# Kernel tuning notes

Hardware: AMD Instinct MI355X
Metric: run time of the kernel (lower is better)

The kernel has to match this reference:

```python
import jax, jax.numpy as jnp
import numpy as np

NB_VEC = 4  # module init arg nbVec
TEMP = 20.0  # distance temperature in exp(-d/20)


def setup_inputs() -> dict:
    key = jax.random.key(0)
    k1, k2 = jax.random.split(key)
    B, C, H, W = 16, 64, 256, 256
    x = jax.random.normal(k1, (B, C, H, W), dtype=jnp.float32)
    # stands in for torch.rand score init used when prior is None
    score_init = jax.random.uniform(k2, (B, H * W), dtype=jnp.float32)
    return {"x": x, "score_init": score_init}


def reference(x, score_init):
    B, C, H, W = x.shape
    N = H * W
    # [B, N, C] flattened spatial features
    xf = jnp.transpose(x, (0, 2, 3, 1)).reshape(B, N, C)
    batch = jnp.arange(B)
    score = score_init
    vecs, sims = [], []
    for _ in range(NB_VEC):
        ind = jnp.argmax(score, axis=1)                      # [B] greedy pick
        raw = xf[batch, ind]                                 # [B, C]
        d2 = jnp.sum((xf - raw[:, None, :]) ** 2, axis=-1)   # [B, N]
        # safe sqrt (distance is exactly 0 at the selected pixel)
        sim = jnp.exp(-jnp.sqrt(jnp.maximum(d2, 1e-12)) / TEMP)
        simNorm = sim / jnp.sum(sim, axis=1, keepdims=True)
        reprVec = jnp.einsum('bnc,bn->bc', xf, simNorm)      # softmax-weighted agg
        vecs.append(reprVec)
        sims.append(sim.reshape(B, 1, H, W))
        score = (1.0 - sim) * score                          # suppress nearby pts
    vecList = jnp.stack(vecs, axis=1)                        # [B, nbVec, C]
    simList = jnp.concatenate(sims, axis=1)                  # [B, nbVec, H, W]
    # selectedPos is only incremented in the onlySimSample branch; zeros here
    selectedPos = jnp.zeros((B, 1, H, W), dtype=x.dtype)
    return vecList, simList, selectedPos
```

## Files before the change

### kernel.cpp

```cpp
#include <hip/hip_runtime.h>

#define BB 16
#define CC 64
#define NN 65536
#define NBV 4
#define B64 (BB * 64)


__global__ __launch_bounds__(256)
void k_argmax1(const float* __restrict__ sc_in,
               float* __restrict__ bval, int* __restrict__ bidx,
               float* __restrict__ sel_out) {
    int b = blockIdx.y, blk = blockIdx.x, tid = threadIdx.x;
    const float* s = sc_in + (size_t)b * NN + blk * 1024;
    float v = -1e30f; int vi = 0x7fffffff;
    #pragma unroll
    for (int k = 0; k < 4; k++) {
        int idx = k * 256 + tid;
        float xv = s[idx];
        if (xv > v) { v = xv; vi = blk * 1024 + idx; }
    }
    size_t gt = ((size_t)(b * 64 + blk)) * 256 + tid;
    #pragma unroll
    for (int k = 0; k < 4; k++) sel_out[gt + (size_t)k * 262144] = 0.f;
    __shared__ float sv[256]; __shared__ int si[256];
    sv[tid] = v; si[tid] = vi;
    __syncthreads();
    for (int st = 128; st > 0; st >>= 1) {
        if (tid < st) {
            float ov = sv[tid + st]; int oi = si[tid + st];
            if (ov > sv[tid] || (ov == sv[tid] && oi < si[tid])) { sv[tid] = ov; si[tid] = oi; }
        }
        __syncthreads();
    }
    if (tid == 0) { bval[b * 64 + blk] = sv[0]; bidx[b * 64 + blk] = si[0]; }
}

__global__ __launch_bounds__(256, 2)
void k_iter(const float* __restrict__ x, const float* __restrict__ score_in,
            float* __restrict__ score_out,
            float* __restrict__ bval, int* __restrict__ bidx,
            float* __restrict__ wpart, float* __restrict__ sspart,
            float* __restrict__ sim_out, int iter) {
    int b = blockIdx.y, blk = blockIdx.x, tid = threadIdx.x;
    int lane = tid & 63, wv = tid >> 6;
    __shared__ float raw_s[64];
    __shared__ float4 d2p[2][4][64];

    int rb = (iter & 1) * B64, wb = ((iter & 1) ^ 1) * B64;

    if (tid < 64) {
        float v = bval[rb + b * 64 + tid]; int vi = bidx[rb + b * 64 + tid];
        #pragma unroll
        for (int off = 32; off >= 1; off >>= 1) {
            float ov = __shfl_down(v, off, 64); int oi = __shfl_down(vi, off, 64);
            if (ov > v || (ov == v && oi < vi)) { v = ov; vi = oi; }
        }
        int ind = __shfl(vi, 0, 64);
        raw_s[tid] = x[((size_t)b * 64 + tid) * NN + ind];
    }
    __syncthreads();

    const float* xb = x + ((size_t)b * 64 + wv * 16) * NN;
    float raw[16];
    #pragma unroll
    for (int j = 0; j < 16; j++) raw[j] = raw_s[wv * 16 + j];
    float acc[16];
    #pragma unroll
    for (int j = 0; j < 16; j++) acc[j] = 0.f;

    const size_t sb = (size_t)b * NN;
    const size_t simb = (size_t)(b * NBV + iter) * NN;
    const bool w0 = (wv == 0), upd = (iter < 3);

    float ssacc = 0.f, smax = -1e30f; int smaxi = 0;
    float4 sc_next;
    if (w0 && upd) sc_next = *(const float4*)(score_in + sb + blk * 1024 + lane * 4);

    #pragma unroll 1
    for (int g = 0; g < 4; g++) {
        int n0 = blk * 1024 + g * 256 + lane * 4;
        float4 xv[16];
        #pragma unroll
        for (int j = 0; j < 16; j++) xv[j] = *(const float4*)(xb + (size_t)j * NN + n0);
        float4 sc_cur = sc_next;
        if (w0 && upd && g < 3) sc_next = *(const float4*)(score_in + sb + n0 + 256);
        float4 d2 = make_float4(0.f, 0.f, 0.f, 0.f);
        #pragma unroll
        for (int j = 0; j < 16; j++) {
            float r = raw[j];
            float dx = xv[j].x - r, dy = xv[j].y - r, dz = xv[j].z - r, dw = xv[j].w - r;
            d2.x = fmaf(dx, dx, d2.x); d2.y = fmaf(dy, dy, d2.y);
            d2.z = fmaf(dz, dz, d2.z); d2.w = fmaf(dw, dw, d2.w);
        }
        d2p[g & 1][wv][lane] = d2;
        __syncthreads();
        float4 a0 = d2p[g & 1][0][lane], a1 = d2p[g & 1][1][lane];
        float4 a2 = d2p[g & 1][2][lane], a3 = d2p[g & 1][3][lane];
        float4 sim;
        sim.x = expf(-sqrtf(fmaxf((a0.x + a1.x) + (a2.x + a3.x), 1e-12f)) * 0.05f);
        sim.y = expf(-sqrtf(fmaxf((a0.y + a1.y) + (a2.y + a3.y), 1e-12f)) * 0.05f);
        sim.z = expf(-sqrtf(fmaxf((a0.z + a1.z) + (a2.z + a3.z), 1e-12f)) * 0.05f);
        sim.w = expf(-sqrtf(fmaxf((a0.w + a1.w) + (a2.w + a3.w), 1e-12f)) * 0.05f);
        #pragma unroll
        for (int j = 0; j < 16; j++) {
            acc[j] = fmaf(sim.x, xv[j].x, acc[j]);
            acc[j] = fmaf(sim.y, xv[j].y, acc[j]);
            acc[j] = fmaf(sim.z, xv[j].z, acc[j]);
            acc[j] = fmaf(sim.w, xv[j].w, acc[j]);
        }
        if (w0) {
            ssacc += (sim.x + sim.y) + (sim.z + sim.w);
            *(float4*)(sim_out + simb + n0) = sim;
            if (upd) {
                float4 sc;
                sc.x = sc_cur.x * (1.f - sim.x);
                sc.y = sc_cur.y * (1.f - sim.y);
                sc.z = sc_cur.z * (1.f - sim.z);
                sc.w = sc_cur.w * (1.f - sim.w);
                *(float4*)(score_out + sb + n0) = sc;
                if (sc.x > smax) { smax = sc.x; smaxi = n0; }
                if (sc.y > smax) { smax = sc.y; smaxi = n0 + 1; }
                if (sc.z > smax) { smax = sc.z; smaxi = n0 + 2; }
                if (sc.w > smax) { smax = sc.w; smaxi = n0 + 3; }
            }
        }
    }

    #pragma unroll
    for (int j = 0; j < 16; j++) {
        float v = acc[j];
        #pragma unroll
        for (int off = 32; off >= 1; off >>= 1) v += __shfl_down(v, off, 64);
        if (lane == 0) wpart[(((size_t)b * 64) + blk) * 64 + wv * 16 + j] = v;
    }
    if (w0) {
        float v = ssacc;
        #pragma unroll
        for (int off = 32; off >= 1; off >>= 1) v += __shfl_down(v, off, 64);
        if (lane == 0) sspart[b * 64 + blk] = v;
        if (upd) {
            #pragma unroll
            for (int off = 32; off >= 1; off >>= 1) {
                float ov = __shfl_down(smax, off, 64); int oi = __shfl_down(smaxi, off, 64);
                if (ov > smax || (ov == smax && oi < smaxi)) { smax = ov; smaxi = oi; }
            }
            if (lane == 0) { bval[wb + b * 64 + blk] = smax; bidx[wb + b * 64 + blk] = smaxi; }
        }
    }
}

__global__ void k_fin(const float* __restrict__ wpart, const float* __restrict__ sspart,
                      float* __restrict__ vec_out, int iter) {
    int b = blockIdx.x, tid = threadIdx.x;
    float w = 0.f;
    for (int blk = 0; blk < 64; blk++) w += wpart[(((size_t)b * 64) + blk) * 64 + tid];
    float ss = 0.f;
    for (int blk = 0; blk < 64; blk++) ss += sspart[b * 64 + blk];
    vec_out[(b * NBV + iter) * 64 + tid] = w / ss;
}

extern "C" void kernel_launch(void* const* d_in, const int* in_sizes, int n_in,
                              void* d_out, int out_size, void* d_ws, size_t ws_size,
                              hipStream_t stream) {
    const float* x = (const float*)d_in[0];
    const float* sc_in = (const float*)d_in[1];
    float* out = (float*)d_out;
    float* vec_out = out;
    float* sim_out = vec_out + (size_t)BB * NBV * CC;
    float* sel_out = sim_out + (size_t)BB * NBV * NN;

    float* ws = (float*)d_ws;
    float* score = ws;
    float* bval = ws + (size_t)BB * NN;
    int* bidx = (int*)(bval + 2 * B64);
    float* wpart = bval + 4 * B64;
    float* sspart = wpart + (size_t)BB * 64 * 64;

    k_argmax1<<<dim3(64, BB), 256, 0, stream>>>(sc_in, bval, bidx, sel_out);
    for (int it = 0; it < NBV; it++) {
        const float* s_in = (it == 0) ? sc_in : score;
        k_iter<<<dim3(64, BB), 256, 0, stream>>>(x, s_in, score, bval, bidx,
                                                 wpart, sspart, sim_out, it);
        k_fin<<<dim3(BB), 64, 0, stream>>>(wpart, sspart, vec_out, it);
    }
}
```

Before: 548.1 us.

## Give each wave all 64 channels over fewer pixels and widen partial reductions

The iteration kernel now assigns each wave a strip of 128 pixels with all 64 channels held in registers, so distances are computed entirely within a thread and the shared-memory cross-wave d2 exchange and per-group barriers disappear. The grid doubles to 128 blocks per batch, and partial argmax, weight and sum results go up to 512 partitions per batch. The argmax-seeding kernel and the finalize kernel are reworked to produce and consume the larger partition count. The change removes synchronisation and raises parallelism, but each thread now holds 128 floats of x plus 64 accumulators, which may push register pressure and lower occupancy. It also adds 64 wave shuffle reductions per wave and a larger final reduction.

```diff
diff --git a/kernel.cpp b/kernel.cpp
--- a/kernel.cpp
+++ b/kernel.cpp
@@ -4,7 +4,8 @@
 #define CC 64
 #define NN 65536
 #define NBV 4
-#define B64 (BB * 64)
+#define NPART 512
+#define BP (BB * NPART)
 
 
 __global__ __launch_bounds__(256)
@@ -12,28 +13,20 @@
                float* __restrict__ bval, int* __restrict__ bidx,
                float* __restrict__ sel_out) {
     int b = blockIdx.y, blk = blockIdx.x, tid = threadIdx.x;
-    const float* s = sc_in + (size_t)b * NN + blk * 1024;
-    float v = -1e30f; int vi = 0x7fffffff;
+    int lane = tid & 63, wv = tid >> 6;
+    int n0 = blk * 512 + tid * 2;
+    const float* s = sc_in + (size_t)b * NN;
+    float v0 = s[n0], v1 = s[n0 + 1];
+    float v = v0; int vi = n0;
+    if (v1 > v) { v = v1; vi = n0 + 1; }
+    sel_out[(size_t)b * NN + n0] = 0.f;
+    sel_out[(size_t)b * NN + n0 + 1] = 0.f;
     #pragma unroll
-    for (int k = 0; k < 4; k++) {
-        int idx = k * 256 + tid;
-        float xv = s[idx];
-        if (xv > v) { v = xv; vi = blk * 1024 + idx; }
+    for (int off = 32; off >= 1; off >>= 1) {
+        float ov = __shfl_down(v, off, 64); int oi = __shfl_down(vi, off, 64);
+        if (ov > v || (ov == v && oi < vi)) { v = ov; vi = oi; }
     }
-    size_t gt = ((size_t)(b * 64 + blk)) * 256 + tid;
-    #pragma unroll
-    for (int k = 0; k < 4; k++) sel_out[gt + (size_t)k * 262144] = 0.f;
-    __shared__ float sv[256]; __shared__ int si[256];
-    sv[tid] = v; si[tid] = vi;
-    __syncthreads();
-    for (int st = 128; st > 0; st >>= 1) {
-        if (tid < st) {
-            float ov = sv[tid + st]; int oi = si[tid + st];
-            if (ov > sv[tid] || (ov == sv[tid] && oi < si[tid])) { sv[tid] = ov; si[tid] = oi; }
-        }
-        __syncthreads();
-    }
-    if (tid == 0) { bval[b * 64 + blk] = sv[0]; bidx[b * 64 + blk] = si[0]; }
+    if (lane == 0) { bval[b * NPART + blk * 4 + wv] = v; bidx[b * NPART + blk * 4 + wv] = vi; }
 }
 
 __global__ __launch_bounds__(256, 2)
@@ -44,120 +37,111 @@
             float* __restrict__ sim_out, int iter) {
     int b = blockIdx.y, blk = blockIdx.x, tid = threadIdx.x;
     int lane = tid & 63, wv = tid >> 6;
+    __shared__ float sv[256]; __shared__ int si[256];
     __shared__ float raw_s[64];
-    __shared__ float4 d2p[2][4][64];
 
-    int rb = (iter & 1) * B64, wb = ((iter & 1) ^ 1) * B64;
+    int rb = (iter & 1) * BP, wb = ((iter & 1) ^ 1) * BP;
 
-    if (tid < 64) {
-        float v = bval[rb + b * 64 + tid]; int vi = bidx[rb + b * 64 + tid];
+    {
+        const float* bv = bval + rb + b * NPART;
+        const int*  bi = bidx + rb + b * NPART;
+        float v = bv[tid]; int vi = bi[tid];
+        float v2 = bv[tid + 256]; int vi2 = bi[tid + 256];
+        if (v2 > v || (v2 == v && vi2 < vi)) { v = v2; vi = vi2; }
+        sv[tid] = v; si[tid] = vi;
+        __syncthreads();
+        for (int st = 128; st > 0; st >>= 1) {
+            if (tid < st) {
+                float ov = sv[tid + st]; int oi = si[tid + st];
+                if (ov > sv[tid] || (ov == sv[tid] && oi < si[tid])) { sv[tid] = ov; si[tid] = oi; }
+            }
+            __syncthreads();
+        }
+    }
+    int ind = si[0];
+    if (tid < 64) raw_s[tid] = x[((size_t)(b * 64 + tid)) * NN + ind];
+    __syncthreads();
+
+    int p = blk * 4 + wv;
+    int n0 = blk * 512 + wv * 128 + lane * 2;
+    const float* xb = x + (size_t)b * 64 * NN + n0;
+    const size_t sb = (size_t)b * NN;
+    const bool upd = (iter < 3);
+
+    float2 sc = make_float2(0.f, 0.f);
+    if (upd) sc = *(const float2*)(score_in + sb + n0);
+
+    float2 xv[64];
+    #pragma unroll
+    for (int c = 0; c < 64; c++) xv[c] = *(const float2*)(xb + (size_t)c * NN);
+    float d2x = 0.f, d2y = 0.f;
+    #pragma unroll
+    for (int c = 0; c < 64; c++) {
+        float r = raw_s[c];
+        float dx = xv[c].x - r, dy = xv[c].y - r;
+        d2x = fmaf(dx, dx, d2x); d2y = fmaf(dy, dy, d2y);
+    }
+
+    float simx = expf(-sqrtf(fmaxf(d2x, 1e-12f)) * 0.05f);
+    float simy = expf(-sqrtf(fmaxf(d2y, 1e-12f)) * 0.05f);
+    *(float2*)(sim_out + ((size_t)(b * NBV + iter)) * NN + n0) = make_float2(simx, simy);
+
+    float ss = simx + simy;
+    float smax = -1e30f; int smaxi = 0x7fffffff;
+    if (upd) {
+        float ncx = sc.x * (1.f - simx), ncy = sc.y * (1.f - simy);
+        *(float2*)(score_out + sb + n0) = make_float2(ncx, ncy);
+        smax = ncx; smaxi = n0;
+        if (ncy > smax) { smax = ncy; smaxi = n0 + 1; }
+    }
+
+    float accl[64];
+    #pragma unroll
+    for (int c = 0; c < 64; c++) accl[c] = fmaf(simx, xv[c].x, simy * xv[c].y);
+
+    #pragma unroll
+    for (int c = 0; c < 64; c++) {
+        float v = accl[c];
+        #pragma unroll
+        for (int off = 32; off >= 1; off >>= 1) v += __shfl_down(v, off, 64);
+        if (lane == 0) wpart[((size_t)b * NPART + p) * 64 + c] = v;
+    }
+    #pragma unroll
+    for (int off = 32; off >= 1; off >>= 1) ss += __shfl_down(ss, off, 64);
+    if (lane == 0) sspart[b * NPART + p] = ss;
+    if (upd) {
         #pragma unroll
         for (int off = 32; off >= 1; off >>= 1) {
-            float ov = __shfl_down(v, off, 64); int oi = __shfl_down(vi, off, 64);
-            if (ov > v || (ov == v && oi < vi)) { v = ov; vi = oi; }
+            float ov = __shfl_down(smax, off, 64); int oi = __shfl_down(smaxi, off, 64);
+            if (ov > smax || (ov == smax && oi < smaxi)) { smax = ov; smaxi = oi; }
         }
-        int ind = __shfl(vi, 0, 64);
-        raw_s[tid] = x[((size_t)b * 64 + tid) * NN + ind];
-    }
-    __syncthreads();
-
-    const float* xb = x + ((size_t)b * 64 + wv * 16) * NN;
-    float raw[16];
-    #pragma unroll
-    for (int j = 0; j < 16; j++) raw[j] = raw_s[wv * 16 + j];
-    float acc[16];
-    #pragma unroll
-    for (int j = 0; j < 16; j++) acc[j] = 0.f;
-
-    const size_t sb = (size_t)b * NN;
-    const size_t simb = (size_t)(b * NBV + iter) * NN;
-    const bool w0 = (wv == 0), upd = (iter < 3);
-
-    float ssacc = 0.f, smax = -1e30f; int smaxi = 0;
-    float4 sc_next;
-    if (w0 && upd) sc_next = *(const float4*)(score_in + sb + blk * 1024 + lane * 4);
-
-    #pragma unroll 1
-    for (int g = 0; g < 4; g++) {
-        int n0 = blk * 1024 + g * 256 + lane * 4;
-        float4 xv[16];
-        #pragma unroll
-        for (int j = 0; j < 16; j++) xv[j] = *(const float4*)(xb + (size_t)j * NN + n0);
-        float4 sc_cur = sc_next;
-        if (w0 && upd && g < 3) sc_next = *(const float4*)(score_in + sb + n0 + 256);
-        float4 d2 = make_float4(0.f, 0.f, 0.f, 0.f);
-        #pragma unroll
-        for (int j = 0; j < 16; j++) {
-            float r = raw[j];
-            float dx = xv[j].x - r, dy = xv[j].y - r, dz = xv[j].z - r, dw = xv[j].w - r;
-            d2.x = fmaf(dx, dx, d2.x); d2.y = fmaf(dy, dy, d2.y);
-            d2.z = fmaf(dz, dz, d2.z); d2.w = fmaf(dw, dw, d2.w);
-        }
-        d2p[g & 1][wv][lane] = d2;
-        __syncthreads();
-        float4 a0 = d2p[g & 1][0][lane], a1 = d2p[g & 1][1][lane];
-        float4 a2 = d2p[g & 1][2][lane], a3 = d2p[g & 1][3][lane];
-        float4 sim;
-        sim.x = expf(-sqrtf(fmaxf((a0.x + a1.x) + (a2.x + a3.x), 1e-12f)) * 0.05f);
-        sim.y = expf(-sqrtf(fmaxf((a0.y + a1.y) + (a2.y + a3.y), 1e-12f)) * 0.05f);
-        sim.z = expf(-sqrtf(fmaxf((a0.z + a1.z) + (a2.z + a3.z), 1e-12f)) * 0.05f);
-        sim.w = expf(-sqrtf(fmaxf((a0.w + a1.w) + (a2.w + a3.w), 1e-12f)) * 0.05f);
-        #pragma unroll
-        for (int j = 0; j < 16; j++) {
-            acc[j] = fmaf(sim.x, xv[j].x, acc[j]);
-            acc[j] = fmaf(sim.y, xv[j].y, acc[j]);
-            acc[j] = fmaf(sim.z, xv[j].z, acc[j]);
-            acc[j] = fmaf(sim.w, xv[j].w, acc[j]);
-        }
-        if (w0) {
-            ssacc += (sim.x + sim.y) + (sim.z + sim.w);
-            *(float4*)(sim_out + simb + n0) = sim;
-            if (upd) {
-                float4 sc;
-                sc.x = sc_cur.x * (1.f - sim.x);
-                sc.y = sc_cur.y * (1.f - sim.y);
-                sc.z = sc_cur.z * (1.f - sim.z);
-                sc.w = sc_cur.w * (1.f - sim.w);
-                *(float4*)(score_out + sb + n0) = sc;
-                if (sc.x > smax) { smax = sc.x; smaxi = n0; }
-                if (sc.y > smax) { smax = sc.y; smaxi = n0 + 1; }
-                if (sc.z > smax) { smax = sc.z; smaxi = n0 + 2; }
-                if (sc.w > smax) { smax = sc.w; smaxi = n0 + 3; }
-            }
-        }
-    }
-
-    #pragma unroll
-    for (int j = 0; j < 16; j++) {
-        float v = acc[j];
-        #pragma unroll
-        for (int off = 32; off >= 1; off >>= 1) v += __shfl_down(v, off, 64);
-        if (lane == 0) wpart[(((size_t)b * 64) + blk) * 64 + wv * 16 + j] = v;
-    }
-    if (w0) {
-        float v = ssacc;
-        #pragma unroll
-        for (int off = 32; off >= 1; off >>= 1) v += __shfl_down(v, off, 64);
-        if (lane == 0) sspart[b * 64 + blk] = v;
-        if (upd) {
-            #pragma unroll
-            for (int off = 32; off >= 1; off >>= 1) {
-                float ov = __shfl_down(smax, off, 64); int oi = __shfl_down(smaxi, off, 64);
-                if (ov > smax || (ov == smax && oi < smaxi)) { smax = ov; smaxi = oi; }
-            }
-            if (lane == 0) { bval[wb + b * 64 + blk] = smax; bidx[wb + b * 64 + blk] = smaxi; }
-        }
+        if (lane == 0) { bval[wb + b * NPART + p] = smax; bidx[wb + b * NPART + p] = smaxi; }
     }
 }
 
-__global__ void k_fin(const float* __restrict__ wpart, const float* __restrict__ sspart,
-                      float* __restrict__ vec_out, int iter) {
+__global__ __launch_bounds__(256)
+void k_fin(const float* __restrict__ wpart, const float* __restrict__ sspart,
+           float* __restrict__ vec_out, int iter) {
     int b = blockIdx.x, tid = threadIdx.x;
+    int c = tid & 63, q = tid >> 6;
+    __shared__ float lw[4][64];
+    __shared__ float lss[256];
+    lss[tid] = sspart[b * NPART + 2 * tid] + sspart[b * NPART + 2 * tid + 1];
     float w = 0.f;
-    for (int blk = 0; blk < 64; blk++) w += wpart[(((size_t)b * 64) + blk) * 64 + tid];
-    float ss = 0.f;
-    for (int blk = 0; blk < 64; blk++) ss += sspart[b * 64 + blk];
-    vec_out[(b * NBV + iter) * 64 + tid] = w / ss;
+    for (int i = 0; i < 128; i++) {
+        int pp = q * 128 + i;
+        w += wpart[((size_t)b * NPART + pp) * 64 + c];
+    }
+    lw[q][c] = w;
+    __syncthreads();
+    for (int st = 128; st > 0; st >>= 1) {
+        if (tid < st) lss[tid] += lss[tid + st];
+        __syncthreads();
+    }
+    if (tid < 64) {
+        float tot = (lw[0][tid] + lw[1][tid]) + (lw[2][tid] + lw[3][tid]);
+        vec_out[(b * NBV + iter) * 64 + tid] = tot / lss[0];
+    }
 }
 
 extern "C" void kernel_launch(void* const* d_in, const int* in_sizes, int n_in,
@@ -173,15 +157,15 @@
     float* ws = (float*)d_ws;
     float* score = ws;
     float* bval = ws + (size_t)BB * NN;
-    int* bidx = (int*)(bval + 2 * B64);
-    float* wpart = bval + 4 * B64;
-    float* sspart = wpart + (size_t)BB * 64 * 64;
+    int* bidx = (int*)(bval + 2 * BP);
+    float* wpart = bval + 4 * BP;
+    float* sspart = wpart + (size_t)BP * 64;
 
-    k_argmax1<<<dim3(64, BB), 256, 0, stream>>>(sc_in, bval, bidx, sel_out);
+    k_argmax1<<<dim3(128, BB), 256, 0, stream>>>(sc_in, bval, bidx, sel_out);
     for (int it = 0; it < NBV; it++) {
         const float* s_in = (it == 0) ? sc_in : score;
-        k_iter<<<dim3(64, BB), 256, 0, stream>>>(x, s_in, score, bval, bidx,
-                                                 wpart, sspart, sim_out, it);
-        k_fin<<<dim3(BB), 64, 0, stream>>>(wpart, sspart, vec_out, it);
+        k_iter<<<dim3(128, BB), 256, 0, stream>>>(x, s_in, score, bval, bidx,
+                                                  wpart, sspart, sim_out, it);
+        k_fin<<<dim3(BB), 256, 0, stream>>>(wpart, sspart, vec_out, it);
     }
 }
```

Result: slower. 624.2 us (+13.9%).

## Split pick kernel, widen k_iter to 512 threads with double-buffered x loads

Applied to the files above, without the earlier changes.

Moves the per-iteration argmax reduction and raw-vector gather into a separate small k_pick kernel, so k_iter can start streaming x immediately. k_iter now uses 8 waves of 8 channels each, with register double-buffering that prefetches the next group's x and score while the current group computes. Score update work moves to wave 1 so it runs alongside wave 0's sim writes, and the barrier is replaced by a raw s_barrier with an explicit LDS waitcnt. k_fin is parallelised across 256 threads. In exchange there is one extra kernel launch per iteration, more register pressure from the two x buffers, and an 8-way LDS reduction of partial distances.

```diff
diff --git a/kernel.cpp b/kernel.cpp
--- a/kernel.cpp
+++ b/kernel.cpp
@@ -4,7 +4,8 @@
 #define CC 64
 #define NN 65536
 #define NBV 4
-#define B64 (BB * 64)
+#define NPB 64
+#define BPP (BB * NPB)
 
 
 __global__ __launch_bounds__(256)
@@ -36,128 +37,161 @@
     if (tid == 0) { bval[b * 64 + blk] = sv[0]; bidx[b * 64 + blk] = si[0]; }
 }
 
-__global__ __launch_bounds__(256, 2)
+__global__ void k_pick(const float* __restrict__ x, const float* __restrict__ bval,
+                       const int* __restrict__ bidx, float* __restrict__ rawbuf, int iter) {
+    int b = blockIdx.x, lane = threadIdx.x;
+    int rb = (iter & 1) * BPP;
+    float v = bval[rb + b * 64 + lane]; int vi = bidx[rb + b * 64 + lane];
+    #pragma unroll
+    for (int off = 32; off >= 1; off >>= 1) {
+        float ov = __shfl_down(v, off, 64); int oi = __shfl_down(vi, off, 64);
+        if (ov > v || (ov == v && oi < vi)) { v = ov; vi = oi; }
+    }
+    int ind = __shfl(vi, 0, 64);
+    rawbuf[b * 64 + lane] = x[((size_t)(b * 64 + lane)) * NN + ind];
+}
+
+__global__ __launch_bounds__(512, 4)
 void k_iter(const float* __restrict__ x, const float* __restrict__ score_in,
             float* __restrict__ score_out,
             float* __restrict__ bval, int* __restrict__ bidx,
             float* __restrict__ wpart, float* __restrict__ sspart,
-            float* __restrict__ sim_out, int iter) {
+            float* __restrict__ sim_out, const float* __restrict__ rawbuf, int iter) {
     int b = blockIdx.y, blk = blockIdx.x, tid = threadIdx.x;
     int lane = tid & 63, wv = tid >> 6;
-    __shared__ float raw_s[64];
-    __shared__ float4 d2p[2][4][64];
-
-    int rb = (iter & 1) * B64, wb = ((iter & 1) ^ 1) * B64;
-
-    if (tid < 64) {
-        float v = bval[rb + b * 64 + tid]; int vi = bidx[rb + b * 64 + tid];
-        #pragma unroll
-        for (int off = 32; off >= 1; off >>= 1) {
-            float ov = __shfl_down(v, off, 64); int oi = __shfl_down(vi, off, 64);
-            if (ov > v || (ov == v && oi < vi)) { v = ov; vi = oi; }
-        }
-        int ind = __shfl(vi, 0, 64);
-        raw_s[tid] = x[((size_t)b * 64 + tid) * NN + ind];
-    }
-    __syncthreads();
-
-    const float* xb = x + ((size_t)b * 64 + wv * 16) * NN;
-    float raw[16];
-    #pragma unroll
-    for (int j = 0; j < 16; j++) raw[j] = raw_s[wv * 16 + j];
-    float acc[16];
-    #pragma unroll
-    for (int j = 0; j < 16; j++) acc[j] = 0.f;
-
+    __shared__ __align__(16) float raw_s[64];
+    __shared__ float4 d2p[2][8][64];
+
+    int wb = ((iter & 1) ^ 1) * BPP;
+    if (tid < 64) raw_s[tid] = rawbuf[b * 64 + tid];
+
+    const float* xw = x + ((size_t)(b * 64 + wv * 8)) * NN;
     const size_t sb = (size_t)b * NN;
     const size_t simb = (size_t)(b * NBV + iter) * NN;
-    const bool w0 = (wv == 0), upd = (iter < 3);
-
-    float ssacc = 0.f, smax = -1e30f; int smaxi = 0;
-    float4 sc_next;
-    if (w0 && upd) sc_next = *(const float4*)(score_in + sb + blk * 1024 + lane * 4);
-
-    #pragma unroll 1
-    for (int g = 0; g < 4; g++) {
-        int n0 = blk * 1024 + g * 256 + lane * 4;
-        float4 xv[16];
-        #pragma unroll
-        for (int j = 0; j < 16; j++) xv[j] = *(const float4*)(xb + (size_t)j * NN + n0);
-        float4 sc_cur = sc_next;
-        if (w0 && upd && g < 3) sc_next = *(const float4*)(score_in + sb + n0 + 256);
+    const bool w0 = (wv == 0), w1 = (wv == 1), upd = (iter < 3);
+
+    float acc[8];
+    #pragma unroll
+    for (int j = 0; j < 8; j++) acc[j] = 0.f;
+    float ssacc = 0.f, smax = -1e30f; int smaxi = 0x7fffffff;
+
+    int nb0 = blk * 1024 + lane * 4;
+    float4 xv0[8], xv1[8];
+    #pragma unroll
+    for (int j = 0; j < 8; j++) xv0[j] = *(const float4*)(xw + (size_t)j * NN + nb0);
+    float4 sc0 = make_float4(0.f, 0.f, 0.f, 0.f), sc1 = sc0;
+    if (w1 && upd) sc0 = *(const float4*)(score_in + sb + nb0);
+
+    __syncthreads();
+    float rloc[8];
+    #pragma unroll
+    for (int j = 0; j < 8; j++) rloc[j] = raw_s[wv * 8 + j];
+
+    auto GROUP = [&](int g, float4 (&xc)[8], float4 (&xn)[8], float4& scc, float4& scn) {
+        int ncur = blk * 1024 + g * 256 + lane * 4;
+        if (g < 3) {
+            int nnx = ncur + 256;
+            #pragma unroll
+            for (int j = 0; j < 8; j++) xn[j] = *(const float4*)(xw + (size_t)j * NN + nnx);
+            if (w1 && upd) scn = *(const float4*)(score_in + sb + nnx);
+        }
         float4 d2 = make_float4(0.f, 0.f, 0.f, 0.f);
         #pragma unroll
-        for (int j = 0; j < 16; j++) {
-            float r = raw[j];
-            float dx = xv[j].x - r, dy = xv[j].y - r, dz = xv[j].z - r, dw = xv[j].w - r;
+        for (int j = 0; j < 8; j++) {
+            float r = rloc[j];
+            float dx = xc[j].x - r, dy = xc[j].y - r, dz = xc[j].z - r, dw = xc[j].w - r;
             d2.x = fmaf(dx, dx, d2.x); d2.y = fmaf(dy, dy, d2.y);
             d2.z = fmaf(dz, dz, d2.z); d2.w = fmaf(dw, dw, d2.w);
         }
         d2p[g & 1][wv][lane] = d2;
-        __syncthreads();
-        float4 a0 = d2p[g & 1][0][lane], a1 = d2p[g & 1][1][lane];
-        float4 a2 = d2p[g & 1][2][lane], a3 = d2p[g & 1][3][lane];
+        asm volatile("s_waitcnt lgkmcnt(0)" ::: "memory");
+        __builtin_amdgcn_s_barrier();
+        __builtin_amdgcn_sched_barrier(0);
+        float4 a = d2p[g & 1][0][lane];
+        #pragma unroll
+        for (int w = 1; w < 8; w++) {
+            float4 t = d2p[g & 1][w][lane];
+            a.x += t.x; a.y += t.y; a.z += t.z; a.w += t.w;
+        }
         float4 sim;
-        sim.x = expf(-sqrtf(fmaxf((a0.x + a1.x) + (a2.x + a3.x), 1e-12f)) * 0.05f);
-        sim.y = expf(-sqrtf(fmaxf((a0.y + a1.y) + (a2.y + a3.y), 1e-12f)) * 0.05f);
-        sim.z = expf(-sqrtf(fmaxf((a0.z + a1.z) + (a2.z + a3.z), 1e-12f)) * 0.05f);
-        sim.w = expf(-sqrtf(fmaxf((a0.w + a1.w) + (a2.w + a3.w), 1e-12f)) * 0.05f);
-        #pragma unroll
-        for (int j = 0; j < 16; j++) {
-            acc[j] = fmaf(sim.x, xv[j].x, acc[j]);
-            acc[j] = fmaf(sim.y, xv[j].y, acc[j]);
-            acc[j] = fmaf(sim.z, xv[j].z, acc[j]);
-            acc[j] = fmaf(sim.w, xv[j].w, acc[j]);
+        sim.x = expf(-sqrtf(fmaxf(a.x, 1e-12f)) * 0.05f);
+        sim.y = expf(-sqrtf(fmaxf(a.y, 1e-12f)) * 0.05f);
+        sim.z = expf(-sqrtf(fmaxf(a.z, 1e-12f)) * 0.05f);
+        sim.w = expf(-sqrtf(fmaxf(a.w, 1e-12f)) * 0.05f);
+        #pragma unroll
+        for (int j = 0; j < 8; j++) {
+            acc[j] = fmaf(sim.x, xc[j].x, acc[j]);
+            acc[j] = fmaf(sim.y, xc[j].y, acc[j]);
+            acc[j] = fmaf(sim.z, xc[j].z, acc[j]);
+            acc[j] = fmaf(sim.w, xc[j].w, acc[j]);
         }
         if (w0) {
             ssacc += (sim.x + sim.y) + (sim.z + sim.w);
-            *(float4*)(sim_out + simb + n0) = sim;
-            if (upd) {
-                float4 sc;
-                sc.x = sc_cur.x * (1.f - sim.x);
-                sc.y = sc_cur.y * (1.f - sim.y);
-                sc.z = sc_cur.z * (1.f - sim.z);
-                sc.w = sc_cur.w * (1.f - sim.w);
-                *(float4*)(score_out + sb + n0) = sc;
-                if (sc.x > smax) { smax = sc.x; smaxi = n0; }
-                if (sc.y > smax) { smax = sc.y; smaxi = n0 + 1; }
-                if (sc.z > smax) { smax = sc.z; smaxi = n0 + 2; }
-                if (sc.w > smax) { smax = sc.w; smaxi = n0 + 3; }
-            }
-        }
-    }
-
-    #pragma unroll
-    for (int j = 0; j < 16; j++) {
+            *(float4*)(sim_out + simb + ncur) = sim;
+        }
+        if (w1 && upd) {
+            float4 nc;
+            nc.x = scc.x * (1.f - sim.x);
+            nc.y = scc.y * (1.f - sim.y);
+            nc.z = scc.z * (1.f - sim.z);
+            nc.w = scc.w * (1.f - sim.w);
+            *(float4*)(score_out + sb + ncur) = nc;
+            if (nc.x > smax) { smax = nc.x; smaxi = ncur; }
+            if (nc.y > smax) { smax = nc.y; smaxi = ncur + 1; }
+            if (nc.z > smax) { smax = nc.z; smaxi = ncur + 2; }
+            if (nc.w > smax) { smax = nc.w; smaxi = ncur + 3; }
+        }
+    };
+    GROUP(0, xv0, xv1, sc0, sc1);
+    GROUP(1, xv1, xv0, sc1, sc0);
+    GROUP(2, xv0, xv1, sc0, sc1);
+    GROUP(3, xv1, xv0, sc1, sc0);
+
+    #pragma unroll
+    for (int j = 0; j < 8; j++) {
         float v = acc[j];
         #pragma unroll
         for (int off = 32; off >= 1; off >>= 1) v += __shfl_down(v, off, 64);
-        if (lane == 0) wpart[(((size_t)b * 64) + blk) * 64 + wv * 16 + j] = v;
+        if (lane == 0) wpart[((size_t)(b * 64 + blk)) * 64 + wv * 8 + j] = v;
     }
     if (w0) {
         float v = ssacc;
         #pragma unroll
         for (int off = 32; off >= 1; off >>= 1) v += __shfl_down(v, off, 64);
         if (lane == 0) sspart[b * 64 + blk] = v;
-        if (upd) {
-            #pragma unroll
-            for (int off = 32; off >= 1; off >>= 1) {
-                float ov = __shfl_down(smax, off, 64); int oi = __shfl_down(smaxi, off, 64);
-                if (ov > smax || (ov == smax && oi < smaxi)) { smax = ov; smaxi = oi; }
-            }
-            if (lane == 0) { bval[wb + b * 64 + blk] = smax; bidx[wb + b * 64 + blk] = smaxi; }
-        }
-    }
-}
-
-__global__ void k_fin(const float* __restrict__ wpart, const float* __restrict__ sspart,
-                      float* __restrict__ vec_out, int iter) {
+    }
+    if (w1 && upd) {
+        #pragma unroll
+        for (int off = 32; off >= 1; off >>= 1) {
+            float ov = __shfl_down(smax, off, 64); int oi = __shfl_down(smaxi, off, 64);
+            if (ov > smax || (ov == smax && oi < smaxi)) { smax = ov; smaxi = oi; }
+        }
+        if (lane == 0) { bval[wb + b * 64 + blk] = smax; bidx[wb + b * 64 + blk] = smaxi; }
+    }
+}
+
+__global__ __launch_bounds__(256)
+void k_fin(const float* __restrict__ wpart, const float* __restrict__ sspart,
+           float* __restrict__ vec_out, int iter) {
     int b = blockIdx.x, tid = threadIdx.x;
+    int c = tid & 63, q = tid >> 6;
+    __shared__ float lw[4][64];
+    __shared__ float sstot;
     float w = 0.f;
-    for (int blk = 0; blk < 64; blk++) w += wpart[(((size_t)b * 64) + blk) * 64 + tid];
-    float ss = 0.f;
-    for (int blk = 0; blk < 64; blk++) ss += sspart[b * 64 + blk];
-    vec_out[(b * NBV + iter) * 64 + tid] = w / ss;
+    #pragma unroll
+    for (int i = 0; i < 16; i++) w += wpart[((size_t)(b * 64 + q * 16 + i)) * 64 + c];
+    lw[q][c] = w;
+    if (tid < 64) {
+        float s = sspart[b * 64 + tid];
+        #pragma unroll
+        for (int off = 32; off >= 1; off >>= 1) s += __shfl_down(s, off, 64);
+        if (tid == 0) sstot = s;
+    }
+    __syncthreads();
+    if (tid < 64) {
+        float tot = (lw[0][tid] + lw[1][tid]) + (lw[2][tid] + lw[3][tid]);
+        vec_out[(b * NBV + iter) * 64 + tid] = tot / sstot;
+    }
 }
 
 extern "C" void kernel_launch(void* const* d_in, const int* in_sizes, int n_in,
@@ -173,15 +207,17 @@
     float* ws = (float*)d_ws;
     float* score = ws;
     float* bval = ws + (size_t)BB * NN;
-    int* bidx = (int*)(bval + 2 * B64);
-    float* wpart = bval + 4 * B64;
+    int* bidx = (int*)(bval + 2 * BPP);
+    float* wpart = bval + 4 * BPP;
     float* sspart = wpart + (size_t)BB * 64 * 64;
+    float* rawbuf = sspart + BPP;
 
     k_argmax1<<<dim3(64, BB), 256, 0, stream>>>(sc_in, bval, bidx, sel_out);
     for (int it = 0; it < NBV; it++) {
         const float* s_in = (it == 0) ? sc_in : score;
-        k_iter<<<dim3(64, BB), 256, 0, stream>>>(x, s_in, score, bval, bidx,
-                                                 wpart, sspart, sim_out, it);
-        k_fin<<<dim3(BB), 64, 0, stream>>>(wpart, sspart, vec_out, it);
-    }
-}
+        k_pick<<<dim3(BB), 64, 0, stream>>>(x, bval, bidx, rawbuf, it);
+        k_iter<<<dim3(64, BB), 512, 0, stream>>>(x, s_in, score, bval, bidx,
+                                                 wpart, sspart, sim_out, rawbuf, it);
+        k_fin<<<dim3(BB), 256, 0, stream>>>(wpart, sspart, vec_out, it);
+    }
+}
```

Result: slower. 789.2 us (+44.0%).
